# Kernel optimization log

Hardware: AMD Instinct MI355X
Metric: run time of the kernel (lower is better)

The kernel has to match this reference:

```python
import jax, jax.numpy as jnp
import numpy as np

N = 262144
C = 256
G = 4096  # number of segments (upper bound on group ids)


def setup_inputs() -> dict:
    key = jax.random.key(0)
    ks = jax.random.split(key, 8)
    s = 1.0 / np.sqrt(C)
    x = jax.random.normal(ks[0], (1, N, C), dtype=jnp.float32)
    ix = jax.random.randint(ks[1], (N,), 0, G, dtype=jnp.int64)
    Wf = jax.random.uniform(ks[2], (C, C), jnp.float32, -s, s)
    bf = jax.random.uniform(ks[3], (C,), jnp.float32, -s, s)
    Wg = jax.random.uniform(ks[4], (C, C), jnp.float32, -s, s)
    bg = jax.random.uniform(ks[5], (C,), jnp.float32, -s, s)
    Wh = jax.random.uniform(ks[6], (C, C), jnp.float32, -s, s)
    bh = jax.random.uniform(ks[7], (C,), jnp.float32, -s, s)
    return {"x": x, "Wf": Wf, "bf": bf, "Wg": Wg, "bg": bg, "Wh": Wh, "bh": bh, "ix": ix}


def reference(x, Wf, bf, Wg, bg, Wh, bh, ix):
    # x: [1, N, C]; only batch 0 is used (matches torch module)
    x0 = x[0]                                    # [N, C]
    fx = x0 @ Wf.T + bf                          # [N, C]
    gx = jnp.clip(x0 @ Wg.T + bg, -50.0, 50.0)   # [N, C]
    exp_gx = jnp.exp(gx)                         # [N, C]
    # Segment softmax: sorting + cumsum group relabel in the torch code is
    # mathematically just a per-group normalized weighted sum keyed by ix.
    seg = ix.astype(jnp.int32)
    denom = jax.ops.segment_sum(exp_gx, seg, num_segments=G)   # [G, C]
    w = exp_gx / denom[seg]                                    # [N, C]
    y = jax.ops.segment_sum(fx * w, seg, num_segments=G)       # [G, C]
    y = y @ Wh.T + bh                                          # [G, C]
    out = y[seg]                                               # [N, C]
    return out[None]                                           # [1, N, C]
```

## Files before the change

kernel.cpp:

```cpp
#include <hip/hip_runtime.h>
#include <stdint.h>
#include <stddef.h>

#define N_ROWS 262144
#define CCH    256
#define NGRP   4096

typedef short bf16x8 __attribute__((ext_vector_type(8)));
typedef short bf16x4 __attribute__((ext_vector_type(4)));
typedef float f32x4  __attribute__((ext_vector_type(4)));
typedef float f32x16 __attribute__((ext_vector_type(16)));

static __device__ __forceinline__ short f2bf(float f){
  union { float f; unsigned u; } v; v.f = f;
  unsigned u = v.u;
  unsigned r = (u + 0x7FFFu + ((u >> 16) & 1u)) >> 16;
  return (short)r;
}

typedef __attribute__((address_space(1))) const unsigned int GU32;
typedef __attribute__((address_space(3))) unsigned int LU32;
static __device__ __forceinline__ void gload_lds16(const void* g, void* l){
  __builtin_amdgcn_global_load_lds((GU32*)g, (LU32*)l, 16, 0, 0);
}

__global__ __launch_bounds__(256) void k_castw(
    const float* __restrict__ Wf, const float* __restrict__ Wg,
    const float* __restrict__ Wh,
    short* __restrict__ wfb, short* __restrict__ wgb, float* __restrict__ wht)
{
  int e = blockIdx.x * 256 + threadIdx.x;
  wfb[e] = f2bf(Wf[e]);
  wgb[e] = f2bf(Wg[e]);
  int k = e >> 8, j = e & 255;
  wht[e] = Wh[j * 256 + k];
}

__global__ __launch_bounds__(256) void k_hist(const int* __restrict__ ix, int* __restrict__ counts){
  int i = blockIdx.x * blockDim.x + threadIdx.x;
  int stride = gridDim.x * blockDim.x;
  for (; i < N_ROWS; i += stride) atomicAdd(&counts[ix[i]], 1);
}

__global__ __launch_bounds__(1024) void k_scan(const int* __restrict__ counts, int* __restrict__ cursor){
  __shared__ int sums[1024];
  int t = threadIdx.x;
  int base = t * 4;
  int c0 = counts[base], c1 = counts[base+1], c2 = counts[base+2], c3 = counts[base+3];
  sums[t] = c0 + c1 + c2 + c3;
  __syncthreads();
  for (int off = 1; off < 1024; off <<= 1){
    int v = (t >= off) ? sums[t - off] : 0;
    __syncthreads();
    sums[t] += v;
    __syncthreads();
  }
  int prev = (t == 0) ? 0 : sums[t - 1];
  cursor[base]   = prev;
  cursor[base+1] = prev + c0;
  cursor[base+2] = prev + c0 + c1;
  cursor[base+3] = prev + c0 + c1 + c2;
}

__global__ __launch_bounds__(256) void k_scatter_cast(
    const int* __restrict__ ix, int* __restrict__ cursor,
    const float* __restrict__ x, short* __restrict__ xb,
    int* __restrict__ gid, int* __restrict__ order)
{
  int wave = threadIdx.x >> 6;
  int lane = threadIdx.x & 63;
  int i = blockIdx.x * 4 + wave;
  int stride = gridDim.x * 4;
  for (; i < N_ROWS; i += stride){
    int g = ix[i];
    int p;
    if (lane == 0) p = atomicAdd(&cursor[g], 1);
    p = __shfl(p, 0);
    f32x4 v = *(const f32x4*)(x + (size_t)i * 256 + lane * 4);
    bf16x4 b;
    #pragma unroll
    for (int j = 0; j < 4; ++j) b[j] = f2bf(v[j]);
    *(bf16x4*)(xb + (size_t)p * 256 + lane * 4) = b;
    if (lane == 0){ gid[p] = g; order[p] = i; }
  }
}

__global__ __launch_bounds__(256) void k_gemm(
    const short* __restrict__ xb,
    const short* __restrict__ wfb, const short* __restrict__ wgb,
    const float* __restrict__ bfp, const float* __restrict__ bgp,
    const int* __restrict__ gid,
    float* __restrict__ numer, float* __restrict__ denom)
{
  __shared__ short bst[32][512];

  const int tid  = threadIdx.x;
  const int wave = tid >> 6;
  const int lane = tid & 63;
  const int l31  = lane & 31;
  const int hi   = lane >> 5;

  const int p     = blockIdx.x;
  const int xcd   = p & 7;
  const int ixd   = p >> 3;
  const int cg    = ixd & 7;
  const int bslot = xcd * 32 + (ixd >> 3);
  const int j0    = cg * 32;

  #pragma unroll
  for (int q = 0; q < 8; ++q){
    int f = wave * 8 + q;
    int mat = f >> 4, ks = f & 15;
    const short* wsrc = mat ? wgb : wfb;
    const short* src = wsrc + (size_t)(j0 + l31) * 256 + ks * 16 + hi * 8;
    gload_lds16(src, &bst[f][0]);
  }
  __syncthreads();

  const float bfv = bfp[j0 + l31];
  const float bgv = bgp[j0 + l31];

#define KSTEP(A, KS) do { \
    bf16x8 bF_ = *(const bf16x8*)&bst[(KS)][lane * 8]; \
    accF = __builtin_amdgcn_mfma_f32_32x32x16_bf16((A), bF_, accF, 0, 0, 0); \
    bf16x8 bG_ = *(const bf16x8*)&bst[16 + (KS)][lane * 8]; \
    accG = __builtin_amdgcn_mfma_f32_32x32x16_bf16((A), bG_, accG, 0, 0, 0); \
  } while (0)

  #pragma unroll 1
  for (int tile = bslot; tile < N_ROWS / 128; tile += 256){
    const int row0 = tile * 128 + wave * 32;
    const int gidv = gid[row0 + l31];
    const short* xr = xb + (size_t)(row0 + l31) * 256 + hi * 8;

    f32x16 accF, accG;
    #pragma unroll
    for (int r = 0; r < 16; ++r){ accF[r] = 0.f; accG[r] = 0.f; }

    bf16x8 a0 = *(const bf16x8*)(xr + 0 * 16);
    bf16x8 a1 = *(const bf16x8*)(xr + 1 * 16);
    bf16x8 a2 = *(const bf16x8*)(xr + 2 * 16);
    bf16x8 a3 = *(const bf16x8*)(xr + 3 * 16);
    bf16x8 b0 = *(const bf16x8*)(xr + 4 * 16);
    bf16x8 b1 = *(const bf16x8*)(xr + 5 * 16);
    bf16x8 b2 = *(const bf16x8*)(xr + 6 * 16);
    bf16x8 b3 = *(const bf16x8*)(xr + 7 * 16);
    __builtin_amdgcn_s_setprio(1);
    KSTEP(a0, 0); KSTEP(a1, 1); KSTEP(a2, 2); KSTEP(a3, 3);
    a0 = *(const bf16x8*)(xr + 8 * 16);
    a1 = *(const bf16x8*)(xr + 9 * 16);
    a2 = *(const bf16x8*)(xr + 10 * 16);
    a3 = *(const bf16x8*)(xr + 11 * 16);
    KSTEP(b0, 4); KSTEP(b1, 5); KSTEP(b2, 6); KSTEP(b3, 7);
    b0 = *(const bf16x8*)(xr + 12 * 16);
    b1 = *(const bf16x8*)(xr + 13 * 16);
    b2 = *(const bf16x8*)(xr + 14 * 16);
    b3 = *(const bf16x8*)(xr + 15 * 16);
    KSTEP(a0, 8); KSTEP(a1, 9); KSTEP(a2, 10); KSTEP(a3, 11);
    KSTEP(b0, 12); KSTEP(b1, 13); KSTEP(b2, 14); KSTEP(b3, 15);
    __builtin_amdgcn_s_setprio(0);

    #pragma unroll
    for (int r = 0; r < 16; ++r){
      float g = accG[r] + bgv;
      g = fminf(fmaxf(g, -50.f), 50.f);
      float e = __expf(g);
      accF[r] = (accF[r] + bfv) * e;
      accG[r] = e;
    }

    int gprev = __shfl(gidv, (l31 + 31) & 31);
    bool head = (l31 == 0) || (gidv != gprev);
    unsigned long long hb = __ballot(head) & 0xFFFFFFFFull;
    if (hb == 1ull){
      int g = __shfl(gidv, 0);
      float sF = 0.f, sE = 0.f;
      #pragma unroll
      for (int r = 0; r < 16; ++r){ sF += accF[r]; sE += accG[r]; }
      sF += __shfl_xor(sF, 32);
      sE += __shfl_xor(sE, 32);
      if (hi == 0){
        atomicAdd(&numer[(size_t)g * 256 + j0 + l31], sF);
        atomicAdd(&denom[(size_t)g * 256 + j0 + l31], sE);
      }
    } else {
      int start = 0;
      while (start < 32){
        int g = __shfl(gidv, start);
        unsigned long long rest = hb >> (start + 1);
        int end = rest ? (start + 1 + __builtin_ctzll(rest)) : 32;
        float sF = 0.f, sE = 0.f;
        #pragma unroll
        for (int r = 0; r < 16; ++r){
          int row = (r & 3) + 8 * (r >> 2) + 4 * hi;
          bool in = (row >= start) && (row < end);
          sF += in ? accF[r] : 0.f;
          sE += in ? accG[r] : 0.f;
        }
        sF += __shfl_xor(sF, 32);
        sE += __shfl_xor(sE, 32);
        if (hi == 0){
          atomicAdd(&numer[(size_t)g * 256 + j0 + l31], sF);
          atomicAdd(&denom[(size_t)g * 256 + j0 + l31], sE);
        }
        start = end;
      }
    }
  }
#undef KSTEP
}

__global__ __launch_bounds__(256) void k_yh(
    const float* __restrict__ numer, const float* __restrict__ denom,
    const float* __restrict__ wht, const float* __restrict__ bh,
    float* __restrict__ yh)
{
  __shared__ float ys[16][256];
  int t = threadIdx.x;
  int g0 = blockIdx.x * 16;
  #pragma unroll
  for (int gg = 0; gg < 16; ++gg){
    size_t idx = (size_t)(g0 + gg) * 256 + t;
    float d = denom[idx];
    ys[gg][t] = (d != 0.f) ? (numer[idx] / d) : 0.f;
  }
  __syncthreads();
  float acc[16];
  #pragma unroll
  for (int gg = 0; gg < 16; ++gg) acc[gg] = 0.f;
  for (int k = 0; k < 256; k += 4){
    float w0 = wht[(k+0) * 256 + t];
    float w1 = wht[(k+1) * 256 + t];
    float w2 = wht[(k+2) * 256 + t];
    float w3 = wht[(k+3) * 256 + t];
    #pragma unroll
    for (int gg = 0; gg < 16; ++gg)
      acc[gg] += w0 * ys[gg][k] + w1 * ys[gg][k+1] + w2 * ys[gg][k+2] + w3 * ys[gg][k+3];
  }
  float b = bh[t];
  #pragma unroll
  for (int gg = 0; gg < 16; ++gg) yh[(size_t)(g0 + gg) * 256 + t] = acc[gg] + b;
}

__global__ __launch_bounds__(256) void k_out(const int* __restrict__ order,
    const int* __restrict__ gid, const float* __restrict__ yh, float* __restrict__ out)
{
  int wave = threadIdx.x >> 6;
  int lane = threadIdx.x & 63;
  int pidx = blockIdx.x * 4 + wave;
  int stride = gridDim.x * 4;
  for (; pidx < N_ROWS; pidx += stride){
    int g = gid[pidx];
    int dst = order[pidx];
    f32x4 v = *(const f32x4*)(yh + (size_t)g * 256 + lane * 4);
    *(f32x4*)(out + (size_t)dst * 256 + lane * 4) = v;
  }
}

extern "C" void kernel_launch(void* const* d_in, const int* in_sizes, int n_in,
                              void* d_out, int out_size, void* d_ws, size_t ws_size,
                              hipStream_t stream)
{
  const float* x  = (const float*)d_in[0];
  const float* Wf = (const float*)d_in[1];
  const float* bf = (const float*)d_in[2];
  const float* Wg = (const float*)d_in[3];
  const float* bg = (const float*)d_in[4];
  const float* Wh = (const float*)d_in[5];
  const float* bh = (const float*)d_in[6];
  const int*   ix = (const int*)d_in[7];
  float* out = (float*)d_out;

  char* ws = (char*)d_ws;
  float* numer  = (float*)(ws + 0);
  float* denom  = (float*)(ws + 4194304);
  int*   counts = (int*)  (ws + 8388608);
  int*   cursor = (int*)  (ws + 8404992);
  float* yh     = (float*)(ws + 8421376);
  float* wht    = (float*)(ws + 12615680);
  short* wfb    = (short*)(ws + 12877824);
  short* wgb    = (short*)(ws + 13008896);
  int*   gid    = (int*)  (ws + 13139968);
  int*   order  = (int*)  (ws + 14188544);

  short* xb = (short*)d_out;

  hipMemsetAsync(ws, 0, 8404992, stream);

  k_castw<<<256, 256, 0, stream>>>(Wf, Wg, Wh, wfb, wgb, wht);
  k_hist<<<512, 256, 0, stream>>>(ix, counts);
  k_scan<<<1, 1024, 0, stream>>>(counts, cursor);
  k_scatter_cast<<<2048, 256, 0, stream>>>(ix, cursor, x, xb, gid, order);
  k_gemm<<<2048, 256, 0, stream>>>(xb, wfb, wgb, bf, bg, gid, numer, denom);
  k_yh<<<256, 256, 0, stream>>>(numer, denom, wht, bh, yh);
  k_out<<<2048, 256, 0, stream>>>(order, gid, yh, out);
}
```

Baseline: 722.8 us.

## Store sorted bf16 rows in MFMA-tiled layout and batch per-row atomics

The scatter kernel now has each thread claim a destination slot with its own atomic, stages the source/destination indices in shared memory, and then lets half-waves copy whole rows. The bf16 rows are written in a tiled layout, 32-row tiles split into 16-column k-slices, so that each GEMM wave reads its A fragments from contiguous 1KB chunks instead of strided 512B rows. The aim is to make the A-operand loads in the GEMM coalesced and to spread the atomics over more threads. The grid is halved to one row per thread. The cost is more scattered 16-byte writes during the scatter.

```diff
diff --git a/kernel.cpp b/kernel.cpp
--- a/kernel.cpp
+++ b/kernel.cpp
@@ -23,6 +23,7 @@
 static __device__ __forceinline__ void gload_lds16(const void* g, void* l){
   __builtin_amdgcn_global_load_lds((GU32*)g, (LU32*)l, 16, 0, 0);
 }
+
 
 __global__ __launch_bounds__(256) void k_castw(
     const float* __restrict__ Wf, const float* __restrict__ Wg,
@@ -67,21 +68,36 @@
     const float* __restrict__ x, short* __restrict__ xb,
     int* __restrict__ gid, int* __restrict__ order)
 {
-  int wave = threadIdx.x >> 6;
-  int lane = threadIdx.x & 63;
-  int i = blockIdx.x * 4 + wave;
-  int stride = gridDim.x * 4;
-  for (; i < N_ROWS; i += stride){
-    int g = ix[i];
-    int p;
-    if (lane == 0) p = atomicAdd(&cursor[g], 1);
-    p = __shfl(p, 0);
-    f32x4 v = *(const f32x4*)(x + (size_t)i * 256 + lane * 4);
-    bf16x4 b;
+  __shared__ int p_s[256];
+  __shared__ int i_s[256];
+
+  const int tid  = threadIdx.x;
+  const int wave = tid >> 6;
+  const int lane = tid & 63;
+  const int hl   = lane & 31;
+
+  int i = blockIdx.x * 256 + tid;
+  int g = ix[i];
+  int p = atomicAdd(&cursor[g], 1);
+  gid[p] = g;
+  order[p] = i;
+  p_s[tid] = p;
+  i_s[tid] = i;
+  __syncthreads();
+
+  for (int pass = wave; pass < 128; pass += 4){
+    int slot = pass * 2 + (lane >> 5);
+    int src = i_s[slot];
+    int dst = p_s[slot];
+    const float* xp = x + (size_t)src * 256 + hl * 8;
+    f32x4 v0 = *(const f32x4*)(xp);
+    f32x4 v1 = *(const f32x4*)(xp + 4);
+    bf16x8 b;
     #pragma unroll
-    for (int j = 0; j < 4; ++j) b[j] = f2bf(v[j]);
-    *(bf16x4*)(xb + (size_t)p * 256 + lane * 4) = b;
-    if (lane == 0){ gid[p] = g; order[p] = i; }
+    for (int j = 0; j < 4; ++j){ b[j] = f2bf(v0[j]); b[4+j] = f2bf(v1[j]); }
+    int t  = dst >> 5, r = dst & 31;
+    int ks = hl >> 1, half = hl & 1;
+    *(bf16x8*)(xb + ((size_t)(t * 16 + ks) * 512 + r * 16 + half * 8)) = b;
   }
 }
 
@@ -127,35 +143,37 @@
     accG = __builtin_amdgcn_mfma_f32_32x32x16_bf16((A), bG_, accG, 0, 0, 0); \
   } while (0)
 
+  const int aoff = l31 * 16 + hi * 8;
+
   #pragma unroll 1
   for (int tile = bslot; tile < N_ROWS / 128; tile += 256){
-    const int row0 = tile * 128 + wave * 32;
-    const int gidv = gid[row0 + l31];
-    const short* xr = xb + (size_t)(row0 + l31) * 256 + hi * 8;
+    const int tgrp = tile * 4 + wave;
+    const int gidv = gid[tgrp * 32 + l31];
+    const short* xr = xb + (size_t)tgrp * 8192 + aoff;
 
     f32x16 accF, accG;
     #pragma unroll
     for (int r = 0; r < 16; ++r){ accF[r] = 0.f; accG[r] = 0.f; }
 
-    bf16x8 a0 = *(const bf16x8*)(xr + 0 * 16);
-    bf16x8 a1 = *(const bf16x8*)(xr + 1 * 16);
-    bf16x8 a2 = *(const bf16x8*)(xr + 2 * 16);
-    bf16x8 a3 = *(const bf16x8*)(xr + 3 * 16);
-    bf16x8 b0 = *(const bf16x8*)(xr + 4 * 16);
-    bf16x8 b1 = *(const bf16x8*)(xr + 5 * 16);
-    bf16x8 b2 = *(const bf16x8*)(xr + 6 * 16);
-    bf16x8 b3 = *(const bf16x8*)(xr + 7 * 16);
+    bf16x8 a0 = *(const bf16x8*)(xr + 0 * 512);
+    bf16x8 a1 = *(const bf16x8*)(xr + 1 * 512);
+    bf16x8 a2 = *(const bf16x8*)(xr + 2 * 512);
+    bf16x8 a3 = *(const bf16x8*)(xr + 3 * 512);
+    bf16x8 b0 = *(const bf16x8*)(xr + 4 * 512);
+    bf16x8 b1 = *(const bf16x8*)(xr + 5 * 512);
+    bf16x8 b2 = *(const bf16x8*)(xr + 6 * 512);
+    bf16x8 b3 = *(const bf16x8*)(xr + 7 * 512);
     __builtin_amdgcn_s_setprio(1);
     KSTEP(a0, 0); KSTEP(a1, 1); KSTEP(a2, 2); KSTEP(a3, 3);
-    a0 = *(const bf16x8*)(xr + 8 * 16);
-    a1 = *(const bf16x8*)(xr + 9 * 16);
-    a2 = *(const bf16x8*)(xr + 10 * 16);
-    a3 = *(const bf16x8*)(xr + 11 * 16);
+    a0 = *(const bf16x8*)(xr + 8 * 512);
+    a1 = *(const bf16x8*)(xr + 9 * 512);
+    a2 = *(const bf16x8*)(xr + 10 * 512);
+    a3 = *(const bf16x8*)(xr + 11 * 512);
     KSTEP(b0, 4); KSTEP(b1, 5); KSTEP(b2, 6); KSTEP(b3, 7);
-    b0 = *(const bf16x8*)(xr + 12 * 16);
-    b1 = *(const bf16x8*)(xr + 13 * 16);
-    b2 = *(const bf16x8*)(xr + 14 * 16);
-    b3 = *(const bf16x8*)(xr + 15 * 16);
+    b0 = *(const bf16x8*)(xr + 12 * 512);
+    b1 = *(const bf16x8*)(xr + 13 * 512);
+    b2 = *(const bf16x8*)(xr + 14 * 512);
+    b3 = *(const bf16x8*)(xr + 15 * 512);
     KSTEP(a0, 8); KSTEP(a1, 9); KSTEP(a2, 10); KSTEP(a3, 11);
     KSTEP(b0, 12); KSTEP(b1, 13); KSTEP(b2, 14); KSTEP(b3, 15);
     __builtin_amdgcn_s_setprio(0);
@@ -290,7 +308,7 @@
   k_castw<<<256, 256, 0, stream>>>(Wf, Wg, Wh, wfb, wgb, wht);
   k_hist<<<512, 256, 0, stream>>>(ix, counts);
   k_scan<<<1, 1024, 0, stream>>>(counts, cursor);
-  k_scatter_cast<<<2048, 256, 0, stream>>>(ix, cursor, x, xb, gid, order);
+  k_scatter_cast<<<1024, 256, 0, stream>>>(ix, cursor, x, xb, gid, order);
   k_gemm<<<2048, 256, 0, stream>>>(xb, wfb, wgb, bf, bg, gid, numer, denom);
   k_yh<<<256, 256, 0, stream>>>(numer, denom, wht, bh, yh);
   k_out<<<2048, 256, 0, stream>>>(order, gid, yh, out);
```

New measurement: 805.5 us. +11.4%, slower.
